# Kernel optimization log

Hardware: AMD Instinct MI355X
Metric: run time of the kernel (lower is better)

The kernel has to match this reference:

```python
import jax, jax.numpy as jnp
import numpy as np

N_IN, N_OUT, KNN, N_EL = 100000, 25000, 9, 200000
B, C_IN, C_OUT = 4, 8, 16


def setup_inputs() -> dict:
    key = jax.random.key(0)
    ks = jax.random.split(key, 16)
    M = N_OUT * KNN
    inp = {
        "features": jax.random.normal(ks[0], (B, C_IN, N_IN), jnp.float32),
        "domain_points": jax.random.uniform(ks[1], (N_IN, 2), jnp.float32),
        "range_points": jax.random.uniform(ks[2], (N_OUT, 2), jnp.float32),
        # kNN structure: each range point i has exactly KNN support edges
        "eval_idx_dst": jnp.repeat(jnp.arange(N_OUT, dtype=jnp.int32), KNN),
        "eval_idx_src": jax.random.randint(ks[3], (M,), 0, N_IN, jnp.int32),
        "element_list": jax.random.randint(ks[4], (N_EL, 3), 0, N_IN, jnp.int32),
        # Siren filter MLP: 2 -> 16 x5 -> C_IN*C_OUT (outermost linear)
        "siren_w_in": jax.random.normal(ks[5], (2, 16), jnp.float32) / jnp.sqrt(2.0),
        "siren_b_in": jax.random.normal(ks[6], (16,), jnp.float32) * 0.1,
        "siren_wh": jax.random.normal(ks[7], (4, 16, 16), jnp.float32) / 4.0,
        "siren_bh": jax.random.normal(ks[8], (4, 16), jnp.float32) * 0.1,
        "siren_w_out": jax.random.normal(ks[9], (16, C_IN * C_OUT), jnp.float32) / 4.0,
        "siren_b_out": jax.random.normal(ks[10], (C_IN * C_OUT,), jnp.float32) * 0.1,
        # weight_map: 6 -> 8 -> 8 -> 8 -> 3, all sigmoid
        "wm_w0": jax.random.normal(ks[11], (6, 8), jnp.float32) / jnp.sqrt(6.0),
        "wm_b0": jnp.zeros((8,), jnp.float32),
        "wm_w1": jax.random.normal(ks[12], (8, 8), jnp.float32) / jnp.sqrt(8.0),
        "wm_b1": jnp.zeros((8,), jnp.float32),
        "wm_w2": jax.random.normal(ks[13], (8, 8), jnp.float32) / jnp.sqrt(8.0),
        "wm_b2": jnp.zeros((8,), jnp.float32),
        "wm_w3": jax.random.normal(ks[14], (8, 3), jnp.float32) / jnp.sqrt(8.0),
        "wm_b3": jnp.zeros((3,), jnp.float32),
    }
    return inp


def reference(features, domain_points, range_points, eval_idx_src, eval_idx_dst,
              element_list, siren_w_in, siren_b_in, siren_wh, siren_bh,
              siren_w_out, siren_b_out, wm_w0, wm_b0, wm_w1, wm_b1,
              wm_w2, wm_b2, wm_w3, wm_b3):
    omega_0 = 1.0
    n_in = domain_points.shape[0]
    n_out = range_points.shape[0]
    c_in = features.shape[1]
    c_out = siren_w_out.shape[1] // c_in

    # --- eval_weight_map: per-element MLP + scatter_add to per-node weights ---
    el_pts = domain_points[element_list].reshape(element_list.shape[0], -1)  # [E, 6]
    h = jax.nn.sigmoid(el_pts @ wm_w0 + wm_b0)
    h = jax.nn.sigmoid(h @ wm_w1 + wm_b1)
    h = jax.nn.sigmoid(h @ wm_w2 + wm_b2)
    el_w = jax.nn.sigmoid(h @ wm_w3 + wm_b3)  # [E, 3]
    node_w = jax.ops.segment_sum(el_w.reshape(-1), element_list.reshape(-1),
                                 num_segments=n_in)  # [N_in]
    w = node_w[eval_idx_src]  # [M]

    # --- per-edge Siren filter on relative locations ---
    locs = range_points[eval_idx_dst] - domain_points[eval_idx_src]  # [M, 2]
    h = jnp.sin(omega_0 * (locs @ siren_w_in + siren_b_in))
    for i in range(siren_wh.shape[0]):  # fixed small layer count
        h = jnp.sin(omega_0 * (h @ siren_wh[i] + siren_bh[i]))
    filt = ((h @ siren_w_out + siren_b_out)
            .reshape(-1, c_in, c_out)) / c_in  # [M, C_in, C_out]

    # --- weighted gather -> contract -> scatter (quadrature integral) ---
    gathered = features[:, :, eval_idx_src]  # [B, C_in, M]
    values = jnp.einsum('n,nij,bin->bjn', w, filt, gathered)  # [B, C_out, M]
    seg = jax.ops.segment_sum(values.transpose(2, 0, 1), eval_idx_dst,
                              num_segments=n_out)  # [N_out, B, C_out]
    return seg.transpose(1, 2, 0)  # [B, C_out, N_out]
```

## Files before the change

kernel.cpp:

```cpp
#include <hip/hip_runtime.h>

#define N_IN   100000
#define N_OUT  25000
#define KNN    9
#define N_EL   200000
#define BB     4
#define C_IN   8
#define C_OUT  16
#define M_EDGE (N_OUT * KNN)

#define DPB  28
#define EPB  (DPB * KNN)
#define SOP  65

__global__ void __launch_bounds__(256) elem_kernel(
    const int*   __restrict__ el,
    const float* __restrict__ dp,
    const float* __restrict__ w0, const float* __restrict__ b0,
    const float* __restrict__ w1, const float* __restrict__ b1,
    const float* __restrict__ w2, const float* __restrict__ b2,
    const float* __restrict__ w3, const float* __restrict__ b3,
    float* __restrict__ node_w)
{
    int e = blockIdx.x * 256 + threadIdx.x;
    if (e >= N_EL) return;
    int i0 = el[e*3+0], i1 = el[e*3+1], i2 = el[e*3+2];
    float2 p0 = ((const float2*)dp)[i0];
    float2 p1 = ((const float2*)dp)[i1];
    float2 p2 = ((const float2*)dp)[i2];
    float p[6] = { p0.x, p0.y, p1.x, p1.y, p2.x, p2.y };

    float h[8], h2[8];
#pragma unroll
    for (int k = 0; k < 8; ++k) {
        float t = b0[k];
#pragma unroll
        for (int j = 0; j < 6; ++j) t = fmaf(p[j], w0[j*8+k], t);
        h[k] = 1.f / (1.f + __expf(-t));
    }
#pragma unroll
    for (int k = 0; k < 8; ++k) {
        float t = b1[k];
#pragma unroll
        for (int j = 0; j < 8; ++j) t = fmaf(h[j], w1[j*8+k], t);
        h2[k] = 1.f / (1.f + __expf(-t));
    }
#pragma unroll
    for (int k = 0; k < 8; ++k) {
        float t = b2[k];
#pragma unroll
        for (int j = 0; j < 8; ++j) t = fmaf(h2[j], w2[j*8+k], t);
        h[k] = 1.f / (1.f + __expf(-t));
    }
    float o[3];
#pragma unroll
    for (int k = 0; k < 3; ++k) {
        float t = b3[k];
#pragma unroll
        for (int j = 0; j < 8; ++j) t = fmaf(h[j], w3[j*3+k], t);
        o[k] = 1.f / (1.f + __expf(-t));
    }
    atomicAdd(&node_w[i0], o[0]);
    atomicAdd(&node_w[i1], o[1]);
    atomicAdd(&node_w[i2], o[2]);
}

__global__ void __launch_bounds__(256) transpose_kernel(
    const float* __restrict__ f, float* __restrict__ ft)
{
    int n = blockIdx.x * 256 + threadIdx.x;
    if (n >= N_IN) return;
    float v[32];
#pragma unroll
    for (int c = 0; c < 32; ++c) v[c] = f[c * N_IN + n];
    float4* dst = (float4*)(ft + (size_t)n * 32);
#pragma unroll
    for (int q = 0; q < 8; ++q)
        dst[q] = make_float4(v[q*4], v[q*4+1], v[q*4+2], v[q*4+3]);
}

template <int FT>
__global__ void __launch_bounds__(256) edge_kernel(
    const float* __restrict__ feat,
    const float* __restrict__ dp,
    const float* __restrict__ rp,
    const int*   __restrict__ src_idx,
    const float* __restrict__ node_w,
    const float* __restrict__ w_in,
    const float* __restrict__ b_in,
    const float* __restrict__ wh,
    const float* __restrict__ bh,
    const float* __restrict__ w_out,
    const float* __restrict__ b_out,
    float* __restrict__ out)
{
    __shared__ float s_out[DPB * SOP];
    const int tid = threadIdx.x;

    for (int i = tid; i < DPB * SOP; i += 256) s_out[i] = 0.f;
    __syncthreads();

    const int  e     = blockIdx.x * EPB + tid;
    int        ldst  = tid / KNN;
    const int  dst   = blockIdx.x * DPB + ldst;
    const bool valid = (tid < EPB) && (dst < N_OUT);
    if (!valid) ldst = 0;
    const int  ce    = valid ? e : 0;
    const int  cdst  = valid ? dst : 0;
    const int  src   = src_idx[ce];

    float g[32];
    if (FT) {
        const float4* fp = (const float4*)(feat + (size_t)src * 32);
#pragma unroll
        for (int q = 0; q < 8; ++q) {
            float4 v = fp[q];
            g[q*4+0] = v.x; g[q*4+1] = v.y; g[q*4+2] = v.z; g[q*4+3] = v.w;
        }
    } else {
#pragma unroll
        for (int c = 0; c < 32; ++c) g[c] = feat[c * N_IN + src];
    }
    const float wn    = node_w[src];
    const float scale = valid ? wn * 0.125f : 0.f;

    const float2 rpt = ((const float2*)rp)[cdst];
    const float2 dpt = ((const float2*)dp)[src];
    const float lx = rpt.x - dpt.x;
    const float ly = rpt.y - dpt.y;

    float h[16], h2[16];
#pragma unroll
    for (int k = 0; k < 16; ++k)
        h[k] = __sinf(fmaf(lx, w_in[k], fmaf(ly, w_in[16+k], b_in[k])));

#pragma unroll
    for (int L = 0; L < 4; ++L) {
#pragma unroll
        for (int k = 0; k < 16; ++k) h2[k] = bh[L*16 + k];
#pragma unroll
        for (int j = 0; j < 16; ++j) {
            const float hj = h[j];
#pragma unroll
            for (int k = 0; k < 16; ++k)
                h2[k] = fmaf(hj, wh[L*256 + j*16 + k], h2[k]);
        }
#pragma unroll
        for (int k = 0; k < 16; ++k) h[k] = __sinf(h2[k]);
    }

    float acc[BB * 16];
#pragma unroll
    for (int t = 0; t < BB * 16; ++t) acc[t] = 0.f;
#pragma unroll
    for (int i = 0; i < C_IN; ++i) {
#pragma unroll
        for (int j = 0; j < 16; ++j) {
            float f = b_out[i*16 + j];
#pragma unroll
            for (int k = 0; k < 16; ++k)
                f = fmaf(h[k], w_out[k*128 + i*16 + j], f);
#pragma unroll
            for (int b = 0; b < BB; ++b)
                acc[b*16 + j] = fmaf(f, g[b*8 + i], acc[b*16 + j]);
        }
    }

#pragma unroll
    for (int t = 0; t < BB * 16; ++t)
        atomicAdd(&s_out[ldst * SOP + t], acc[t] * scale);
    __syncthreads();

    const int dst0 = blockIdx.x * DPB;
    for (int i = tid; i < DPB * 64; i += 256) {
        const int d = i % DPB;
        const int c = i / DPB;
        const int gdst = dst0 + d;
        if (gdst < N_OUT)
            out[(size_t)c * N_OUT + gdst] = s_out[d * SOP + c];
    }
}

extern "C" void kernel_launch(void* const* d_in, const int* in_sizes, int n_in,
                              void* d_out, int out_size, void* d_ws, size_t ws_size,
                              hipStream_t stream)
{
    (void)in_sizes; (void)n_in; (void)out_size;
    const float* features = (const float*)d_in[0];
    const float* dp       = (const float*)d_in[1];
    const float* rp       = (const float*)d_in[2];
    const int*   src_idx  = (const int*)d_in[4];
    const int*   el       = (const int*)d_in[5];
    const float* w_in     = (const float*)d_in[6];
    const float* b_in     = (const float*)d_in[7];
    const float* wh       = (const float*)d_in[8];
    const float* bh       = (const float*)d_in[9];
    const float* w_out    = (const float*)d_in[10];
    const float* b_out    = (const float*)d_in[11];
    const float* wm_w0    = (const float*)d_in[12];
    const float* wm_b0    = (const float*)d_in[13];
    const float* wm_w1    = (const float*)d_in[14];
    const float* wm_b1    = (const float*)d_in[15];
    const float* wm_w2    = (const float*)d_in[16];
    const float* wm_b2    = (const float*)d_in[17];
    const float* wm_w3    = (const float*)d_in[18];
    const float* wm_b3    = (const float*)d_in[19];
    float* out = (float*)d_out;

    float*  node_w   = (float*)d_ws;
    size_t  off      = ((size_t)N_IN * sizeof(float) + 511) & ~(size_t)511;
    float*  feat_t   = (float*)((char*)d_ws + off);
    size_t  need_t   = off + (size_t)N_IN * 32 * sizeof(float);
    const bool use_t = (ws_size >= need_t);

    hipMemsetAsync(node_w, 0, (size_t)N_IN * sizeof(float), stream);

    elem_kernel<<<(N_EL + 255) / 256, 256, 0, stream>>>(
        el, dp, wm_w0, wm_b0, wm_w1, wm_b1, wm_w2, wm_b2, wm_w3, wm_b3, node_w);

    if (use_t) {
        transpose_kernel<<<(N_IN + 255) / 256, 256, 0, stream>>>(features, feat_t);
        edge_kernel<1><<<(N_OUT + DPB - 1) / DPB, 256, 0, stream>>>(
            feat_t, dp, rp, src_idx, node_w,
            w_in, b_in, wh, bh, w_out, b_out, out);
    } else {
        edge_kernel<0><<<(N_OUT + DPB - 1) / DPB, 256, 0, stream>>>(
            features, dp, rp, src_idx, node_w,
            w_in, b_in, wh, bh, w_out, b_out, out);
    }
}
```

Baseline: 279.2 us.

## Interleave transposed features by batch, stream feature loads, fold scale, transpose w_out

The transposed feature layout now groups the four batch values per input channel, so the edge kernel loads one float4 per channel inside the contraction loop instead of holding all 32 gathered features in registers. The per-edge scale is folded into the filter value before accumulation, and w_out is pre-transposed so each output column's 16 weights are contiguous. Zeroing node_w moves into the prep kernel, which replaces a memset. A launch-bounds occupancy hint of 4 is added. The aim is lower register pressure and better occupancy, at the cost of an extra ordering dependency and possible spills under the tighter register budget.

New measurement: 295.7 us. +5.9%, slower.

```diff
diff --git a/kernel.cpp b/kernel.cpp
--- a/kernel.cpp
+++ b/kernel.cpp
@@ -65,22 +65,27 @@
     atomicAdd(&node_w[i2], o[2]);
 }
 
-__global__ void __launch_bounds__(256) transpose_kernel(
-    const float* __restrict__ f, float* __restrict__ ft)
+__global__ void __launch_bounds__(256) prep_kernel(
+    const float* __restrict__ f, float* __restrict__ ft,
+    const float* __restrict__ w_out, float* __restrict__ w_out_t,
+    float* __restrict__ node_w)
 {
     int n = blockIdx.x * 256 + threadIdx.x;
+    if (n < C_IN * C_OUT * 16)
+        w_out_t[n] = w_out[(n & 15) * 128 + (n >> 4)];
     if (n >= N_IN) return;
+    node_w[n] = 0.f;
     float v[32];
 #pragma unroll
     for (int c = 0; c < 32; ++c) v[c] = f[c * N_IN + n];
     float4* dst = (float4*)(ft + (size_t)n * 32);
 #pragma unroll
     for (int q = 0; q < 8; ++q)
-        dst[q] = make_float4(v[q*4], v[q*4+1], v[q*4+2], v[q*4+3]);
+        dst[q] = make_float4(v[q], v[8+q], v[16+q], v[24+q]);
 }
 
 template <int FT>
-__global__ void __launch_bounds__(256) edge_kernel(
+__global__ void __launch_bounds__(256, 4) edge_kernel(
     const float* __restrict__ feat,
     const float* __restrict__ dp,
     const float* __restrict__ rp,
@@ -91,6 +96,7 @@
     const float* __restrict__ wh,
     const float* __restrict__ bh,
     const float* __restrict__ w_out,
+    const float* __restrict__ w_out_t,
     const float* __restrict__ b_out,
     float* __restrict__ out)
 {
@@ -109,18 +115,6 @@
     const int  cdst  = valid ? dst : 0;
     const int  src   = src_idx[ce];
 
-    float g[32];
-    if (FT) {
-        const float4* fp = (const float4*)(feat + (size_t)src * 32);
-#pragma unroll
-        for (int q = 0; q < 8; ++q) {
-            float4 v = fp[q];
-            g[q*4+0] = v.x; g[q*4+1] = v.y; g[q*4+2] = v.z; g[q*4+3] = v.w;
-        }
-    } else {
-#pragma unroll
-        for (int c = 0; c < 32; ++c) g[c] = feat[c * N_IN + src];
-    }
     const float wn    = node_w[src];
     const float scale = valid ? wn * 0.125f : 0.f;
 
@@ -152,23 +146,37 @@
     float acc[BB * 16];
 #pragma unroll
     for (int t = 0; t < BB * 16; ++t) acc[t] = 0.f;
+
+    const float4* fp4 = (const float4*)(feat + (size_t)src * 32);
 #pragma unroll
     for (int i = 0; i < C_IN; ++i) {
+        float4 gb;
+        if (FT) {
+            gb = fp4[i];
+        } else {
+            gb = make_float4(feat[(0*8+i) * N_IN + src],
+                             feat[(1*8+i) * N_IN + src],
+                             feat[(2*8+i) * N_IN + src],
+                             feat[(3*8+i) * N_IN + src]);
+        }
 #pragma unroll
         for (int j = 0; j < 16; ++j) {
-            float f = b_out[i*16 + j];
+            const int col = i*16 + j;
+            float f = b_out[col];
 #pragma unroll
             for (int k = 0; k < 16; ++k)
-                f = fmaf(h[k], w_out[k*128 + i*16 + j], f);
-#pragma unroll
-            for (int b = 0; b < BB; ++b)
-                acc[b*16 + j] = fmaf(f, g[b*8 + i], acc[b*16 + j]);
+                f = fmaf(h[k], FT ? w_out_t[col*16 + k] : w_out[k*128 + col], f);
+            f *= scale;
+            acc[0*16 + j] = fmaf(f, gb.x, acc[0*16 + j]);
+            acc[1*16 + j] = fmaf(f, gb.y, acc[1*16 + j]);
+            acc[2*16 + j] = fmaf(f, gb.z, acc[2*16 + j]);
+            acc[3*16 + j] = fmaf(f, gb.w, acc[3*16 + j]);
         }
     }
 
 #pragma unroll
     for (int t = 0; t < BB * 16; ++t)
-        atomicAdd(&s_out[ldst * SOP + t], acc[t] * scale);
+        atomicAdd(&s_out[ldst * SOP + t], acc[t]);
     __syncthreads();
 
     const int dst0 = blockIdx.x * DPB;
@@ -207,25 +215,29 @@
     const float* wm_b3    = (const float*)d_in[19];
     float* out = (float*)d_out;
 
-    float*  node_w   = (float*)d_ws;
-    size_t  off      = ((size_t)N_IN * sizeof(float) + 511) & ~(size_t)511;
-    float*  feat_t   = (float*)((char*)d_ws + off);
-    size_t  need_t   = off + (size_t)N_IN * 32 * sizeof(float);
-    const bool use_t = (ws_size >= need_t);
-
-    hipMemsetAsync(node_w, 0, (size_t)N_IN * sizeof(float), stream);
-
-    elem_kernel<<<(N_EL + 255) / 256, 256, 0, stream>>>(
-        el, dp, wm_w0, wm_b0, wm_w1, wm_b1, wm_w2, wm_b2, wm_w3, wm_b3, node_w);
+    size_t off0 = 0;
+    size_t off1 = (off0 + (size_t)N_IN * sizeof(float) + 511) & ~(size_t)511;
+    size_t off2 = (off1 + (size_t)N_IN * 32 * sizeof(float) + 511) & ~(size_t)511;
+    size_t need = off2 + (size_t)2048 * sizeof(float);
+    float* node_w  = (float*)((char*)d_ws + off0);
+    float* feat_t  = (float*)((char*)d_ws + off1);
+    float* w_out_t = (float*)((char*)d_ws + off2);
+    const bool use_t = (ws_size >= need);
 
     if (use_t) {
-        transpose_kernel<<<(N_IN + 255) / 256, 256, 0, stream>>>(features, feat_t);
+        prep_kernel<<<(N_IN + 255) / 256, 256, 0, stream>>>(
+            features, feat_t, w_out, w_out_t, node_w);
+        elem_kernel<<<(N_EL + 255) / 256, 256, 0, stream>>>(
+            el, dp, wm_w0, wm_b0, wm_w1, wm_b1, wm_w2, wm_b2, wm_w3, wm_b3, node_w);
         edge_kernel<1><<<(N_OUT + DPB - 1) / DPB, 256, 0, stream>>>(
             feat_t, dp, rp, src_idx, node_w,
-            w_in, b_in, wh, bh, w_out, b_out, out);
+            w_in, b_in, wh, bh, w_out, w_out_t, b_out, out);
     } else {
+        hipMemsetAsync(node_w, 0, (size_t)N_IN * sizeof(float), stream);
+        elem_kernel<<<(N_EL + 255) / 256, 256, 0, stream>>>(
+            el, dp, wm_w0, wm_b0, wm_w1, wm_b1, wm_w2, wm_b2, wm_w3, wm_b3, node_w);
         edge_kernel<0><<<(N_OUT + DPB - 1) / DPB, 256, 0, stream>>>(
             features, dp, rp, src_idx, node_w,
-            w_in, b_in, wh, bh, w_out, b_out, out);
-    }
-}
+            w_in, b_in, wh, bh, w_out, (const float*)nullptr, b_out, out);
+    }
+}
```
